# Performance work log

Measured on AMD Instinct MI355X. Metric: run time of the kernel, lower is better.

The kernel has to match this reference:

```python
import jax, jax.numpy as jnp
import numpy as np
import math

B, T, C, H = 2, 2048, 768, 12
HD = C // H
EPS = 1e-5

def setup_inputs() -> dict:
    key = jax.random.key(0)
    ks = jax.random.split(key, 12)
    s = lambda n: 1.0 / math.sqrt(n)
    return {
        "x": jax.random.normal(ks[0], (B, T, C), jnp.float32),
        "ln1_g": jnp.ones((C,), jnp.float32),
        "ln1_b": jnp.zeros((C,), jnp.float32),
        "w_attn": jax.random.normal(ks[1], (C, 3 * C), jnp.float32) * s(C),
        "b_attn": jnp.zeros((3 * C,), jnp.float32),
        "w_proj": jax.random.normal(ks[2], (C, C), jnp.float32) * s(C),
        "b_proj": jnp.zeros((C,), jnp.float32),
        "ln2_g": jnp.ones((C,), jnp.float32),
        "ln2_b": jnp.zeros((C,), jnp.float32),
        "w_fc": jax.random.normal(ks[3], (C, 4 * C), jnp.float32) * s(C),
        "b_fc": jnp.zeros((4 * C,), jnp.float32),
        "w_fc2": jax.random.normal(ks[4], (4 * C, C), jnp.float32) * s(4 * C),
        "b_fc2": jnp.zeros((C,), jnp.float32),
    }

def layernorm(x, g, b):
    mu = jnp.mean(x, axis=-1, keepdims=True)
    var = jnp.mean(jnp.square(x - mu), axis=-1, keepdims=True)
    return (x - mu) * jax.lax.rsqrt(var + EPS) * g + b

def new_gelu(x):
    c = math.sqrt(2.0 / math.pi)
    return 0.5 * x * (1.0 + jnp.tanh(c * (x + 0.044715 * x ** 3)))

def reference(x, ln1_g, ln1_b, w_attn, b_attn, w_proj, b_proj,
              ln2_g, ln2_b, w_fc, b_fc, w_fc2, b_fc2):
    # --- attention branch ---
    h = layernorm(x, ln1_g, ln1_b)
    qkv = h @ w_attn + b_attn                       # [B,T,3C]
    q, k, v = jnp.split(qkv, 3, axis=-1)
    q = q.reshape(B, T, H, HD).transpose(0, 2, 1, 3)  # [B,H,T,hd]
    k = k.reshape(B, T, H, HD).transpose(0, 2, 1, 3)
    v = v.reshape(B, T, H, HD).transpose(0, 2, 1, 3)
    att = jnp.einsum('bhqd,bhkd->bhqk', q, k) * (1.0 / math.sqrt(HD))
    causal = jnp.tril(jnp.ones((T, T), bool))
    att = jnp.where(causal, att, -jnp.inf)
    att = jax.nn.softmax(att, axis=-1)
    y = jnp.einsum('bhqk,bhkd->bhqd', att, v)       # [B,H,T,hd]
    y = y.transpose(0, 2, 1, 3).reshape(B, T, C)
    x = x + y @ w_proj + b_proj
    # --- MLP branch ---
    h2 = layernorm(x, ln2_g, ln2_b)
    x = x + new_gelu(h2 @ w_fc + b_fc) @ w_fc2 + b_fc2
    return x
```

## Files before the change

kernel.cpp:

```cpp
#include <hip/hip_runtime.h>
#include <hip/hip_bf16.h>
#include <math.h>

typedef __hip_bfloat16 bf16;
typedef __attribute__((ext_vector_type(8))) short short8;
typedef __attribute__((ext_vector_type(4))) float floatx4;
typedef __attribute__((ext_vector_type(4))) unsigned uintx4;

#define GLDS16(g, l) __builtin_amdgcn_global_load_lds( \
    (const __attribute__((address_space(1))) void*)(g), \
    (__attribute__((address_space(3))) void*)(l), 16, 0, 0)

__device__ __forceinline__ bf16 f2bf(float v) { return __float2bfloat16(v); }

__device__ __forceinline__ unsigned cvtpk(float a, float b) {
  unsigned r;
  asm volatile("v_cvt_pk_bf16_f32 %0, %1, %2" : "=v"(r) : "v"(a), "v"(b));
  return r;
}

__global__ __launch_bounds__(256) void kconvT(const float* __restrict__ w,
                                              bf16* __restrict__ wT,
                                              int K, int N) {
  __shared__ float tile[32][33];
  const int n0 = blockIdx.x * 32, k0 = blockIdx.y * 32;
  const int tc = threadIdx.x & 31, tr = threadIdx.x >> 5;
#pragma unroll
  for (int p = 0; p < 4; p++)
    tile[tr + p * 8][tc] = w[(size_t)(k0 + tr + p * 8) * N + n0 + tc];
  __syncthreads();
#pragma unroll
  for (int p = 0; p < 4; p++)
    wT[(size_t)(n0 + tr + p * 8) * K + k0 + tc] = f2bf(tile[tc][tr + p * 8]);
}

__global__ __launch_bounds__(256) void kln(const float* __restrict__ x,
                                           const float* __restrict__ gw,
                                           const float* __restrict__ bw,
                                           bf16* __restrict__ out) {
  const int row = blockIdx.x, tid = threadIdx.x;
  const float* xr = x + (size_t)row * 768;
  float v0 = xr[tid], v1 = xr[tid + 256], v2 = xr[tid + 512];
  float s = v0 + v1 + v2;
  float s2 = v0 * v0 + v1 * v1 + v2 * v2;
#pragma unroll
  for (int off = 1; off < 64; off <<= 1) {
    s += __shfl_xor(s, off);
    s2 += __shfl_xor(s2, off);
  }
  __shared__ float red[8];
  const int wid = tid >> 6, lane = tid & 63;
  if (lane == 0) { red[wid] = s; red[4 + wid] = s2; }
  __syncthreads();
  s = red[0] + red[1] + red[2] + red[3];
  s2 = red[4] + red[5] + red[6] + red[7];
  const float mu = s * (1.f / 768.f);
  const float rst = rsqrtf(fmaxf(s2 * (1.f / 768.f) - mu * mu, 0.f) + 1e-5f);
  bf16* orow = out + (size_t)row * 768;
  orow[tid] = f2bf((v0 - mu) * rst * gw[tid] + bw[tid]);
  orow[tid + 256] = f2bf((v1 - mu) * rst * gw[tid + 256] + bw[tid + 256]);
  orow[tid + 512] = f2bf((v2 - mu) * rst * gw[tid + 512] + bw[tid + 512]);
}

__global__ __launch_bounds__(256) void kxpose(const bf16* __restrict__ qkv,
                                              bf16* __restrict__ VT) {
  const int T = 2048, C3 = 2304;
  const int t0 = blockIdx.x * 64, h = blockIdx.y, b = blockIdx.z;
  const int tid = threadIdx.x;
  __shared__ short tile[64][66];
  const bf16* src = qkv + (size_t)b * T * C3 + 1536 + h * 64;
  const int tr = tid >> 3, c = tid & 7;
#pragma unroll
  for (int p = 0; p < 2; p++) {
    short8 v = *(const short8*)(src + (size_t)(t0 + tr + p * 32) * C3 + c * 8);
    *(short8*)&tile[tr + p * 32][c * 8] = v;
  }
  __syncthreads();
  bf16* dst = VT + ((size_t)(b * 12 + h) * 64) * T + t0;
#pragma unroll
  for (int p = 0; p < 2; p++) {
    const int d = (tid >> 3) + p * 32, tc = tid & 7;
    short8 v;
#pragma unroll
    for (int j = 0; j < 8; j++) v[j] = tile[tc * 8 + j][d];
    *(short8*)(dst + (size_t)d * T + tc * 8) = v;
  }
}

template <int BN, int EPI>
__global__ __launch_bounds__(256, 2) void kgemm(
    const bf16* __restrict__ A, const bf16* __restrict__ BT,
    const float* __restrict__ bias, const float* __restrict__ resid,
    bf16* __restrict__ outb, float* __restrict__ outf, int M, int N, int K) {
  __shared__ bf16 As[128 * 32];
  __shared__ bf16 Bs[BN * 32];
  const int tid = threadIdx.x;
  const int wid = tid >> 6, lane = tid & 63, g = lane >> 4, q = lane & 15;
  constexpr int FM = (BN == 128) ? 4 : 2;
  constexpr int FN = 4;
  constexpr int WM = (BN == 128) ? 64 : 32;
  const int wr = (BN == 128) ? (wid >> 1) : wid;
  const int wc = (BN == 128) ? (wid & 1) : 0;
  const int row0 = blockIdx.y * 128, col0 = blockIdx.x * BN;
  floatx4 acc[FM][FN] = {};
  const int r0 = tid >> 2;
  const int c0 = (tid & 3) * 8;
  const bf16* Ab = A + (size_t)row0 * K;
  const bf16* Bb = BT + (size_t)col0 * K;

  for (int k0 = 0; k0 < K; k0 += 32) {
    GLDS16(Ab + (size_t)r0 * K + k0 + c0, (char*)As + wid * 1024);
    GLDS16(Ab + (size_t)(r0 + 64) * K + k0 + c0, (char*)As + 4096 + wid * 1024);
    GLDS16(Bb + (size_t)r0 * K + k0 + c0, (char*)Bs + wid * 1024);
    if constexpr (BN == 128)
      GLDS16(Bb + (size_t)(r0 + 64) * K + k0 + c0, (char*)Bs + 4096 + wid * 1024);
    __syncthreads();
    short8 af[FM], bfr[FN];
#pragma unroll
    for (int m = 0; m < FM; m++)
      af[m] = *(const short8*)&As[(wr * WM + m * 16 + q) * 32 + g * 8];
#pragma unroll
    for (int n = 0; n < FN; n++)
      bfr[n] = *(const short8*)&Bs[(wc * 64 + n * 16 + q) * 32 + g * 8];
#pragma unroll
    for (int m = 0; m < FM; m++)
#pragma unroll
      for (int n = 0; n < FN; n++)
        acc[m][n] =
            __builtin_amdgcn_mfma_f32_16x16x32_bf16(af[m], bfr[n], acc[m][n], 0, 0, 0);
    __syncthreads();
  }

#pragma unroll
  for (int n = 0; n < FN; n++) {
    const int col = col0 + wc * 64 + n * 16 + q;
    const float bv = bias[col];
#pragma unroll
    for (int m = 0; m < FM; m++) {
      const int rowb = row0 + wr * WM + m * 16 + g * 4;
#pragma unroll
      for (int r = 0; r < 4; r++) {
        const size_t idx = (size_t)(rowb + r) * N + col;
        const float v = acc[m][n][r] + bv;
        if (EPI == 0) {
          outb[idx] = f2bf(v);
        } else if (EPI == 1) {
          outf[idx] = v + resid[idx];
        } else {
          const float t = tanhf(0.7978845608028654f * (v + 0.044715f * v * v * v));
          outb[idx] = f2bf(0.5f * v * (1.0f + t));
        }
      }
    }
  }
}

__global__ __launch_bounds__(256, 2) void kattn(const bf16* __restrict__ qkv,
                                                const bf16* __restrict__ VT,
                                                bf16* __restrict__ y) {
  const int T = 2048, C3 = 2304;
  const int tid = threadIdx.x;
  const int w = tid >> 6, lane = tid & 63;
  const int g = lane >> 4, qi = lane & 15;

  const int bid = blockIdx.x;
  const int lb = (bid & 7) * 96 + (bid >> 3);
  const int qblk = 31 - (lb & 31);
  const int h = (lb >> 5) % 12, b = (lb >> 5) / 12;
  const int q0w = qblk * 64 + w * 16;
  const int qrow = q0w + qi;

  const bf16* Qb = qkv + (size_t)b * T * C3 + h * 64;
  const char* Ksrc = (const char*)(Qb + 768);
  const char* Vsrc = (const char*)(VT + (size_t)(b * 12 + h) * 64 * T);

  __shared__ __align__(16) char smem[32768];

  const int nt = qblk + 1;

  short8 qf[2];
#pragma unroll
  for (int s = 0; s < 2; s++)
    qf[s] = *(const short8*)(Qb + (size_t)qrow * C3 + s * 32 + g * 8);

  const int kvb = (qi >> 2) * 8 + (qi & 3);
  const unsigned swz = (unsigned)(((lane & 7) ^ (lane >> 3)) << 4);
  const int srow = lane >> 3;

  float m_run = -1e30f, l_run = 0.f;
  floatx4 o[4] = {};

#define STAGE(t)                                                                   \
  {                                                                                \
    char* base_ = smem + ((t) & 1) * 16384;                                        \
    const int kv0_ = (t) * 64;                                                     \
    _Pragma("unroll")                                                              \
    for (int j = 0; j < 2; j++) {                                                  \
      const int c_ = w * 2 + j;                                                    \
      GLDS16(Ksrc + (size_t)(kv0_ + c_ * 8 + srow) * 4608 + swz, base_ + c_ * 1024); \
      GLDS16(Vsrc + (size_t)(c_ * 8 + srow) * 4096 + kv0_ * 2 + swz,               \
             base_ + 8192 + c_ * 1024);                                            \
    }                                                                              \
  }

  STAGE(0);
  asm volatile("s_waitcnt vmcnt(0)");
  __syncthreads();

  for (int t = 0; t < nt; t++) {
    if (t + 1 < nt) STAGE(t + 1);
    const char* Kl = smem + (t & 1) * 16384;
    const char* Vl = Kl + 8192;
    const int kv0 = t * 64;

    short8 kf[8];
#pragma unroll
    for (int c = 0; c < 4; c++) {
      const int R = kvb + (c & 1) * 4 + (c >> 1) * 32;
#pragma unroll
      for (int s = 0; s < 2; s++)
        kf[c * 2 + s] =
            *(const short8*)(Kl + R * 128 + (((s * 4 + g) ^ (R & 7)) << 4));
    }
    short8 vfr[8];
#pragma unroll
    for (int ks = 0; ks < 2; ks++)
#pragma unroll
      for (int n = 0; n < 4; n++) {
        const int R2 = n * 16 + qi;
        vfr[ks * 4 + n] =
            *(const short8*)(Vl + R2 * 128 + (((ks * 4 + g) ^ (R2 & 7)) << 4));
      }

    floatx4 sacc[4] = {};
#pragma unroll
    for (int c = 0; c < 4; c++)
#pragma unroll
      for (int s = 0; s < 2; s++)
        sacc[c] =
            __builtin_amdgcn_mfma_f32_16x16x32_bf16(kf[c * 2 + s], qf[s], sacc[c], 0, 0, 0);

    if (kv0 + 63 > q0w) {
#pragma unroll
      for (int c = 0; c < 4; c++)
#pragma unroll
        for (int r = 0; r < 4; r++) {
          const int kv = kv0 + g * 8 + (c & 1) * 4 + r + (c >> 1) * 32;
          if (kv > qrow) sacc[c][r] = -1e30f;
        }
    }
    float mx = sacc[0][0];
#pragma unroll
    for (int c = 0; c < 4; c++)
#pragma unroll
      for (int r = 0; r < 4; r++) mx = fmaxf(mx, sacc[c][r]);
    mx = fmaxf(mx, __shfl_xor(mx, 16));
    mx = fmaxf(mx, __shfl_xor(mx, 32));
    mx *= 0.125f;
    const float mn = fmaxf(m_run, mx);
    const float al = __expf(m_run - mn);
    float ps = 0.f;
    unsigned pk[8];
#pragma unroll
    for (int c = 0; c < 4; c++) {
      float p0 = __expf(fmaf(sacc[c][0], 0.125f, -mn));
      float p1 = __expf(fmaf(sacc[c][1], 0.125f, -mn));
      float p2 = __expf(fmaf(sacc[c][2], 0.125f, -mn));
      float p3 = __expf(fmaf(sacc[c][3], 0.125f, -mn));
      ps += (p0 + p1) + (p2 + p3);
      pk[c * 2] = cvtpk(p0, p1);
      pk[c * 2 + 1] = cvtpk(p2, p3);
    }
    ps += __shfl_xor(ps, 16);
    ps += __shfl_xor(ps, 32);
    l_run = l_run * al + ps;
    m_run = mn;
#pragma unroll
    for (int n = 0; n < 4; n++) o[n] *= al;

#pragma unroll
    for (int ks = 0; ks < 2; ks++) {
      uintx4 pu;
      pu.x = pk[ks * 4 + 0];
      pu.y = pk[ks * 4 + 1];
      pu.z = pk[ks * 4 + 2];
      pu.w = pk[ks * 4 + 3];
      const short8 pf = __builtin_bit_cast(short8, pu);
#pragma unroll
      for (int n = 0; n < 4; n++)
        o[n] = __builtin_amdgcn_mfma_f32_16x16x32_bf16(vfr[ks * 4 + n], pf, o[n], 0, 0, 0);
    }

    asm volatile("s_waitcnt vmcnt(0)");
    __syncthreads();
  }
#undef STAGE

  const float inv = 1.0f / l_run;
  bf16* yr = y + (size_t)(b * T + qrow) * 768 + h * 64;
#pragma unroll
  for (int n = 0; n < 4; n++) {
    uint2 pr;
    pr.x = cvtpk(o[n][0] * inv, o[n][1] * inv);
    pr.y = cvtpk(o[n][2] * inv, o[n][3] * inv);
    *(uint2*)(yr + n * 16 + g * 4) = pr;
  }
}

extern "C" void kernel_launch(void* const* d_in, const int* in_sizes, int n_in,
                              void* d_out, int out_size, void* d_ws, size_t ws_size,
                              hipStream_t stream) {
  const float* x      = (const float*)d_in[0];
  const float* ln1_g  = (const float*)d_in[1];
  const float* ln1_b  = (const float*)d_in[2];
  const float* w_attn = (const float*)d_in[3];
  const float* b_attn = (const float*)d_in[4];
  const float* w_proj = (const float*)d_in[5];
  const float* b_proj = (const float*)d_in[6];
  const float* ln2_g  = (const float*)d_in[7];
  const float* ln2_b  = (const float*)d_in[8];
  const float* w_fc   = (const float*)d_in[9];
  const float* b_fc   = (const float*)d_in[10];
  const float* w_fc2  = (const float*)d_in[11];
  const float* b_fc2  = (const float*)d_in[12];
  float* out = (float*)d_out;

  const int M = 4096;
  char* p = (char*)d_ws;
  bf16* wT_attn = (bf16*)p; p += (size_t)2304 * 768 * 2;
  bf16* wT_proj = (bf16*)p; p += (size_t)768 * 768 * 2;
  bf16* wT_fc   = (bf16*)p; p += (size_t)3072 * 768 * 2;
  bf16* wT_fc2  = (bf16*)p; p += (size_t)768 * 3072 * 2;
  bf16* h       = (bf16*)p; p += (size_t)M * 768 * 2;
  bf16* qkv     = (bf16*)p;
  bf16* yb      = (bf16*)(p + (size_t)M * 2304 * 2);
  bf16* act     = qkv;      p += (size_t)M * 2304 * 2 + (size_t)M * 768 * 2;
  float* x1     = (float*)p;
  bf16* VT      = (bf16*)p;

  kconvT<<<dim3(2304 / 32, 768 / 32), 256, 0, stream>>>(w_attn, wT_attn, 768, 2304);
  kconvT<<<dim3(768 / 32, 768 / 32), 256, 0, stream>>>(w_proj, wT_proj, 768, 768);
  kconvT<<<dim3(3072 / 32, 768 / 32), 256, 0, stream>>>(w_fc, wT_fc, 768, 3072);
  kconvT<<<dim3(768 / 32, 3072 / 32), 256, 0, stream>>>(w_fc2, wT_fc2, 3072, 768);

  kln<<<M, 256, 0, stream>>>(x, ln1_g, ln1_b, h);
  kgemm<128, 0><<<dim3(2304 / 128, M / 128), 256, 0, stream>>>(
      h, wT_attn, b_attn, nullptr, qkv, nullptr, M, 2304, 768);
  kxpose<<<dim3(32, 12, 2), 256, 0, stream>>>(qkv, VT);
  kattn<<<dim3(768), 256, 0, stream>>>(qkv, VT, yb);
  kgemm<64, 1><<<dim3(768 / 64, M / 128), 256, 0, stream>>>(
      yb, wT_proj, b_proj, x, nullptr, x1, M, 768, 768);

  kln<<<M, 256, 0, stream>>>(x1, ln2_g, ln2_b, h);
  kgemm<128, 2><<<dim3(3072 / 128, M / 128), 256, 0, stream>>>(
      h, wT_fc, b_fc, nullptr, act, nullptr, M, 3072, 768);
  kgemm<64, 1><<<dim3(768 / 64, M / 128), 256, 0, stream>>>(
      act, wT_fc2, b_fc2, x1, nullptr, out, M, 768, 3072);
}
```

Baseline: 224.7 us.

## Double-buffer GEMM LDS tiles and XOR-swizzle columns to avoid bank conflicts

The GEMM kernel now keeps two LDS buffers per operand and issues the global-to-LDS loads for the next K tile before computing on the current one. This lets memory latency overlap with MFMA work and drops one barrier per iteration. It also applies an XOR swizzle to the 16-byte chunk position, on both the load side and the fragment-read side, to reduce LDS bank conflicts. The cost is twice the LDS per block, which could reduce occupancy, and an explicit vmcnt wait per iteration.

```diff
diff --git a/kernel.cpp b/kernel.cpp
--- a/kernel.cpp
+++ b/kernel.cpp
@@ -92,8 +92,8 @@
     const bf16* __restrict__ A, const bf16* __restrict__ BT,
     const float* __restrict__ bias, const float* __restrict__ resid,
     bf16* __restrict__ outb, float* __restrict__ outf, int M, int N, int K) {
-  __shared__ bf16 As[128 * 32];
-  __shared__ bf16 Bs[BN * 32];
+  __shared__ bf16 As[2][128 * 32];
+  __shared__ bf16 Bs[2][BN * 32];
   const int tid = threadIdx.x;
   const int wid = tid >> 6, lane = tid & 63, g = lane >> 4, q = lane & 15;
   constexpr int FM = (BN == 128) ? 4 : 2;
@@ -104,30 +104,44 @@
   const int row0 = blockIdx.y * 128, col0 = blockIdx.x * BN;
   floatx4 acc[FM][FN] = {};
   const int r0 = tid >> 2;
-  const int c0 = (tid & 3) * 8;
+  const int c0 = (((tid & 3) ^ ((r0 >> 1) & 3))) * 8;
+  const int lsl = (g ^ ((q >> 1) & 3)) * 16;
   const bf16* Ab = A + (size_t)row0 * K;
   const bf16* Bb = BT + (size_t)col0 * K;
 
-  for (int k0 = 0; k0 < K; k0 += 32) {
-    GLDS16(Ab + (size_t)r0 * K + k0 + c0, (char*)As + wid * 1024);
-    GLDS16(Ab + (size_t)(r0 + 64) * K + k0 + c0, (char*)As + 4096 + wid * 1024);
-    GLDS16(Bb + (size_t)r0 * K + k0 + c0, (char*)Bs + wid * 1024);
+  auto STAGE = [&](int kk, int buf) {
+    GLDS16(Ab + (size_t)r0 * K + kk + c0, (char*)&As[buf][0] + wid * 1024);
+    GLDS16(Ab + (size_t)(r0 + 64) * K + kk + c0,
+           (char*)&As[buf][0] + 4096 + wid * 1024);
+    GLDS16(Bb + (size_t)r0 * K + kk + c0, (char*)&Bs[buf][0] + wid * 1024);
     if constexpr (BN == 128)
-      GLDS16(Bb + (size_t)(r0 + 64) * K + k0 + c0, (char*)Bs + 4096 + wid * 1024);
-    __syncthreads();
+      GLDS16(Bb + (size_t)(r0 + 64) * K + kk + c0,
+             (char*)&Bs[buf][0] + 4096 + wid * 1024);
+  };
+
+  const int nk = K >> 5;
+  STAGE(0, 0);
+  asm volatile("s_waitcnt vmcnt(0)");
+  __syncthreads();
+
+  for (int kt = 0; kt < nk; kt++) {
+    if (kt + 1 < nk) STAGE((kt + 1) << 5, (kt + 1) & 1);
+    const char* Ac = (const char*)&As[kt & 1][0];
+    const char* Bc = (const char*)&Bs[kt & 1][0];
     short8 af[FM], bfr[FN];
 #pragma unroll
     for (int m = 0; m < FM; m++)
-      af[m] = *(const short8*)&As[(wr * WM + m * 16 + q) * 32 + g * 8];
+      af[m] = *(const short8*)(Ac + (wr * WM + m * 16 + q) * 64 + lsl);
 #pragma unroll
     for (int n = 0; n < FN; n++)
-      bfr[n] = *(const short8*)&Bs[(wc * 64 + n * 16 + q) * 32 + g * 8];
+      bfr[n] = *(const short8*)(Bc + (wc * 64 + n * 16 + q) * 64 + lsl);
 #pragma unroll
     for (int m = 0; m < FM; m++)
 #pragma unroll
       for (int n = 0; n < FN; n++)
         acc[m][n] =
             __builtin_amdgcn_mfma_f32_16x16x32_bf16(af[m], bfr[n], acc[m][n], 0, 0, 0);
+    asm volatile("s_waitcnt vmcnt(0)");
     __syncthreads();
   }
 
```

Result: faster. 212.9 us (-5.2%).
